# Kernel optimization log

Measured on AMD Instinct MI355X. Metric: run time of the kernel, lower is better.

The kernel has to match this reference:

```python
import jax, jax.numpy as jnp
import numpy as np

H = 128   # hidden_size
C = 80    # number of classes / per-class GRUs


def setup_inputs():
    key = jax.random.key(0)
    ks = jax.random.split(key, 16)
    lengths = np.array([100 + 4 * j for j in range(C)], dtype=np.int64)   # ragged segment sizes
    ucl = np.concatenate([np.zeros(1, np.int64), np.cumsum(lengths)])     # [C+1] boundaries
    N = int(ucl[-1])                                                      # 20640 total boxes
    r = jax.random.normal
    return {
        "boxes_feature": r(ks[0], (N, 1024), jnp.float32),
        "boxes_score": r(ks[1], (N, 32), jnp.float32),
        "boxes_box": r(ks[2], (N, 4), jnp.float32),
        "all_class_boxes_feature": r(ks[3], (N, 1024), jnp.float32),
        "all_class_boxes_score": r(ks[4], (N, 32), jnp.float32),
        "all_class_boxes_box": r(ks[5], (N, 32), jnp.float32),
        "all_class_boxes_origin_score": r(ks[6], (N, 32), jnp.float32),
        "unique_class": np.ones(C, dtype=np.int64),
        "unique_class_len": ucl,
        "appear_W": r(ks[7], (H, 1024), jnp.float32) / np.sqrt(1024.0).astype(np.float32),
        "appear_b": jnp.zeros((H,), jnp.float32),
        "feat_W": r(ks[8], (H, H + 96), jnp.float32) / np.sqrt(float(H + 96)).astype(np.float32),
        "feat_b": jnp.zeros((H,), jnp.float32),
        "gru_Wih": r(ks[9], (C, 2, 3 * H, H), jnp.float32) / np.sqrt(float(H)).astype(np.float32),
        "gru_Whh": r(ks[10], (C, 2, 3 * H, H), jnp.float32) / np.sqrt(float(H)).astype(np.float32),
        "gru_bih": r(ks[11], (C, 2, 3 * H), jnp.float32) * 0.01,
        "gru_bhh": r(ks[12], (C, 2, 3 * H), jnp.float32) * 0.01,
        "out_W": r(ks[13], (1, 2 * H), jnp.float32) / np.sqrt(2.0 * H).astype(np.float32),
        "out_b": jnp.zeros((1,), jnp.float32),
    }


def _forward(all_class_boxes_feature, all_class_boxes_score, all_class_boxes_box,
             all_class_boxes_origin_score, unique_class, unique_class_len,
             appear_W, appear_b, feat_W, feat_b,
             gru_Wih, gru_Whh, gru_bih, gru_bhh, out_W, out_b):
    # --- static ragged bookkeeping (int inputs are concrete numpy) ---
    ucl = np.asarray(unique_class_len)
    lengths = ucl[1:] - ucl[:-1]                                   # [C]
    starts = ucl[:-1]
    L = int(lengths.max())
    t = np.arange(L)
    mask = jnp.asarray(t[None, :] < lengths[:, None])              # [C,L] valid-position mask
    gidx = jnp.asarray(starts[:, None] + np.minimum(t[None, :], lengths[:, None] - 1))  # [C,L]
    ridx = jnp.asarray(np.clip(lengths[:, None] - 1 - t[None, :], 0, None))             # [C,L]

    # --- shared feature pipeline ---
    feat = jax.nn.relu(all_class_boxes_feature @ appear_W.T + appear_b)   # [N,H]
    allf = jnp.concatenate([feat, all_class_boxes_score, all_class_boxes_box,
                            all_class_boxes_origin_score], axis=1)        # [N,H+96]
    dec = jax.nn.relu(allf @ feat_W.T + feat_b)                           # [N,H]

    X = dec[gidx]                                                  # [C,L,H] padded per-class segments
    Xr = jnp.take_along_axis(X, ridx[:, :, None], axis=1)          # time-reversed within each length

    def run_dir(Xd, Wih, Whh, bih, bhh):
        # precompute input projections; scan only carries the hidden recurrence
        Xp = jnp.einsum('clh,cgh->clg', Xd, Wih) + bih[:, None, :]  # [C,L,3H]

        def per_class(xp, m, Whh_c, bhh_c):
            def step(h, inp):
                x_t, m_t = inp
                gh = Whh_c @ h + bhh_c
                r = jax.nn.sigmoid(x_t[:H] + gh[:H])                # PyTorch gate order r,z,n
                z = jax.nn.sigmoid(x_t[H:2 * H] + gh[H:2 * H])
                n = jnp.tanh(x_t[2 * H:] + r * gh[2 * H:])
                h2 = jnp.where(m_t, (1.0 - z) * n + z * h, h)
                return h2, h2
            _, out = jax.lax.scan(step, jnp.zeros((H,), xp.dtype), (xp, m))
            return out                                              # [L,H]
        return jax.vmap(per_class)(Xp, mask, Whh, bhh)              # [C,L,H]

    out_f = run_dir(X, gru_Wih[:, 0], gru_Whh[:, 0], gru_bih[:, 0], gru_bhh[:, 0])
    out_r = run_dir(Xr, gru_Wih[:, 1], gru_Whh[:, 1], gru_bih[:, 1], gru_bhh[:, 1])
    out_bd = jnp.take_along_axis(out_r, ridx[:, :, None], axis=1)   # un-reverse backward outputs
    Y = jnp.concatenate([out_f, out_bd], axis=-1)                   # [C,L,2H]

    # flatten valid positions back to the original box order (segments are contiguous)
    seg = jnp.asarray(np.repeat(np.arange(C), lengths))
    loc = jnp.asarray(np.concatenate([np.arange(int(l)) for l in lengths]))
    flat = Y[seg, loc]                                              # [N,2H]
    return jax.nn.sigmoid(flat @ out_W.T + out_b)[:, None, :]       # [N,1,1] like torch output


def reference(boxes_feature, boxes_score, boxes_box, all_class_boxes_feature,
              all_class_boxes_score, all_class_boxes_box, all_class_boxes_origin_score,
              unique_class, unique_class_len, appear_W, appear_b, feat_W, feat_b,
              gru_Wih, gru_Whh, gru_bih, gru_bhh, out_W, out_b):
    # boxes_feature/boxes_score/boxes_box are accepted but unused, as in the torch forward
    return _forward(all_class_boxes_feature, all_class_boxes_score, all_class_boxes_box,
                    all_class_boxes_origin_score, unique_class, unique_class_len,
                    appear_W, appear_b, feat_W, feat_b,
                    gru_Wih, gru_Whh, gru_bih, gru_bhh, out_W, out_b)
```

## Files before the change

kernel.cpp:

```cpp
#include <hip/hip_runtime.h>
#include <hip/hip_bf16.h>
#include <cstdint>


typedef _Float16 half2_t __attribute__((ext_vector_type(2)));
typedef _Float16 half8_t __attribute__((ext_vector_type(8)));
typedef float f32x4 __attribute__((ext_vector_type(4)));

__device__ __forceinline__ void lds_barrier() {
    asm volatile("s_waitcnt lgkmcnt(0)\n\ts_barrier" ::: "memory");
}

__device__ __forceinline__ half8_t cvt8(float4 f0, float4 f1) {
    return half8_t{(_Float16)f0.x, (_Float16)f0.y, (_Float16)f0.z, (_Float16)f0.w,
                   (_Float16)f1.x, (_Float16)f1.y, (_Float16)f1.z, (_Float16)f1.w};
}

__global__ __launch_bounds__(256) void concat_kernel(
    const float* __restrict__ score, const float* __restrict__ box,
    const float* __restrict__ orig, _Float16* __restrict__ allf, int N)
{
    int idx = blockIdx.x * 256 + threadIdx.x;
    int total = N * 96;
    if (idx >= total) return;
    int n = idx / 96, j = idx - n * 96;
    float v;
    if (j < 32)      v = score[(size_t)n * 32 + j];
    else if (j < 64) v = box  [(size_t)n * 32 + j - 32];
    else             v = orig [(size_t)n * 32 + j - 64];
    allf[(size_t)n * 224 + 128 + j] = (_Float16)v;
}

template<bool A_F16>
__global__ __launch_bounds__(256) void mfma_gemm_kernel(
    const void* __restrict__ Av, int lda,
    const float* __restrict__ B, int ldb,
    const float* __restrict__ bias,
    _Float16* __restrict__ Cc, int ldc,
    int Nrows, int K, int do_relu)
{
    __shared__ __align__(16) _Float16 Asl[256 * 8];
    __shared__ __align__(16) _Float16 Bsl[512 * 8];
    const int tid = threadIdx.x;
    const int wave = tid >> 6, lane = tid & 63;
    const int n0 = blockIdx.x * 64;

    const int a_rt = tid >> 6, a_q = (tid >> 4) & 3, a_m = tid & 15;
    int arow = n0 + a_rt * 16 + a_m; if (arow > Nrows - 1) arow = Nrows - 1;
    const int b_q = (tid >> 4) & 3, b_n = tid & 15;
    const int bcol0 = (tid >> 6) * 16 + b_n;
    const int bcol1 = bcol0 + 64;

    f32x4 acc[8] = {};
    half8_t a_st, b_st0, b_st1;

    auto load_chunk = [&](int kc) {
        int k = kc * 32;
        if constexpr (A_F16) {
            const _Float16* A = (const _Float16*)Av;
            a_st = *(const half8_t*)(A + (size_t)arow * lda + k + a_q * 8);
        } else {
            const float* A = (const float*)Av;
            const float4* p = (const float4*)(A + (size_t)arow * lda + k + a_q * 8);
            a_st = cvt8(p[0], p[1]);
        }
        const float4* p0 = (const float4*)(B + (size_t)bcol0 * ldb + k + b_q * 8);
        const float4* p1 = (const float4*)(B + (size_t)bcol1 * ldb + k + b_q * 8);
        b_st0 = cvt8(p0[0], p0[1]);
        b_st1 = cvt8(p1[0], p1[1]);
    };

    load_chunk(0);
    const int nkc = K >> 5;
    for (int kc = 0; kc < nkc; kc++) {
        lds_barrier();
        *(half8_t*)(Asl + tid * 8) = a_st;
        *(half8_t*)(Bsl + tid * 8) = b_st0;
        *(half8_t*)(Bsl + (tid + 256) * 8) = b_st1;
        lds_barrier();
        if (kc + 1 < nkc) load_chunk(kc + 1);
        half8_t af = *(const half8_t*)(Asl + (wave * 64 + lane) * 8);
        #pragma unroll
        for (int ct = 0; ct < 8; ct++) {
            half8_t bf = *(const half8_t*)(Bsl + (ct * 64 + lane) * 8);
            acc[ct] = __builtin_amdgcn_mfma_f32_16x16x32_f16(af, bf, acc[ct], 0, 0, 0);
        }
    }

    const int crow = n0 + wave * 16 + (lane >> 4) * 4;
    const int ccol = lane & 15;
    #pragma unroll
    for (int ct = 0; ct < 8; ct++) {
        int col = ct * 16 + ccol;
        float bv = bias[col];
        #pragma unroll
        for (int reg = 0; reg < 4; reg++) {
            int row = crow + reg;
            if (row >= Nrows) continue;
            float v = acc[ct][reg] + bv;
            if (do_relu) v = v > 0.f ? v : 0.f;
            Cc[(size_t)row * ldc + col] = (_Float16)v;
        }
    }
}

__global__ __launch_bounds__(256) void mfma_xp_kernel(
    const _Float16* __restrict__ dec,
    const float* __restrict__ Wih,
    const float* __restrict__ bih,
    const int* __restrict__ ucl,
    _Float16* __restrict__ xp,
    int N)
{
    const int c = blockIdx.x;
    const int tile = blockIdx.y;
    const int d = blockIdx.z / 3, mt = blockIdx.z % 3;
    const int start = ucl[c];
    const int len = ucl[c + 1] - start;
    const int t0 = tile * 64;
    if (t0 >= len) return;

    __shared__ __align__(16) _Float16 Asl[256 * 8];
    __shared__ __align__(16) _Float16 Bsl[512 * 8];
    const int tid = threadIdx.x;
    const int wave = tid >> 6, lane = tid & 63;

    const int a_rt = tid >> 6, a_q = (tid >> 4) & 3, a_m = tid & 15;
    int t = t0 + a_rt * 16 + a_m; if (t > len - 1) t = len - 1;
    const int srow = start + (d ? (len - 1 - t) : t);

    const float* Bb = Wih + ((size_t)(c * 2 + d) * 384 + mt * 128) * 128;
    const int b_q = (tid >> 4) & 3, b_n = tid & 15;
    const int bcol0 = (tid >> 6) * 16 + b_n;
    const int bcol1 = bcol0 + 64;

    f32x4 acc[8] = {};
    half8_t a_st, b_st0, b_st1;

    auto load_chunk = [&](int kc) {
        int k = kc * 32;
        a_st = *(const half8_t*)(dec + (size_t)srow * 128 + k + a_q * 8);
        const float4* p0 = (const float4*)(Bb + (size_t)bcol0 * 128 + k + b_q * 8);
        const float4* p1 = (const float4*)(Bb + (size_t)bcol1 * 128 + k + b_q * 8);
        b_st0 = cvt8(p0[0], p0[1]);
        b_st1 = cvt8(p1[0], p1[1]);
    };

    load_chunk(0);
    for (int kc = 0; kc < 4; kc++) {
        lds_barrier();
        *(half8_t*)(Asl + tid * 8) = a_st;
        *(half8_t*)(Bsl + tid * 8) = b_st0;
        *(half8_t*)(Bsl + (tid + 256) * 8) = b_st1;
        lds_barrier();
        if (kc + 1 < 4) load_chunk(kc + 1);
        half8_t af = *(const half8_t*)(Asl + (wave * 64 + lane) * 8);
        #pragma unroll
        for (int ct = 0; ct < 8; ct++) {
            half8_t bf = *(const half8_t*)(Bsl + (ct * 64 + lane) * 8);
            acc[ct] = __builtin_amdgcn_mfma_f32_16x16x32_f16(af, bf, acc[ct], 0, 0, 0);
        }
    }

    const float* bias = bih + (size_t)(c * 2 + d) * 384 + mt * 128;
    const int trow = t0 + wave * 16 + (lane >> 4) * 4;
    const int ccol = lane & 15;
    #pragma unroll
    for (int ct = 0; ct < 8; ct++) {
        int col = ct * 16 + ccol;
        float bv = bias[col];
        #pragma unroll
        for (int reg = 0; reg < 4; reg++) {
            int tt = trow + reg;
            if (tt >= len) continue;
            float v = acc[ct][reg] + bv;
            xp[((size_t)d * N + start + tt) * 384 + mt * 128 + col] = (_Float16)v;
        }
    }
}

__global__ __launch_bounds__(128, 1) void gru_kernel(
    const _Float16* __restrict__ xp,
    const float* __restrict__ Whh,
    const float* __restrict__ bhh,
    const int* __restrict__ ucl,
    float* __restrict__ outY,
    int N)
{
    const int c = blockIdx.x, d = blockIdx.y;
    const int start = ucl[c];
    const int len = ucl[c + 1] - start;
    const int g = threadIdx.x;

    const float* wbase = Whh + (size_t)(c * 2 + d) * 384 * 128;
    half2_t w0[64], w1[64], w2[64];
    {
        const float2* r0 = (const float2*)(wbase + (size_t)g * 128);
        const float2* r1 = (const float2*)(wbase + (size_t)(g + 128) * 128);
        const float2* r2 = (const float2*)(wbase + (size_t)(g + 256) * 128);
        #pragma unroll
        for (int i = 0; i < 64; i++) {
            float2 a = r0[i];
            w0[i] = half2_t{(_Float16)a.x, (_Float16)a.y};
        }
        #pragma unroll
        for (int i = 0; i < 64; i++) {
            float2 a = r1[i];
            w1[i] = half2_t{(_Float16)a.x, (_Float16)a.y};
        }
        #pragma unroll
        for (int i = 0; i < 64; i++) {
            float2 a = r2[i];
            w2[i] = half2_t{(_Float16)a.x, (_Float16)a.y};
        }
    }
    const float* bb = bhh + (size_t)(c * 2 + d) * 384;
    const float bh0 = bb[g], bh1 = bb[g + 128], bh2 = bb[g + 256];

    __shared__ __align__(16) half2_t hbuf[2][64];
    if (g < 64) { hbuf[0][g] = half2_t{(_Float16)0.f, (_Float16)0.f}; }
    const _Float16* xpb = xp + ((size_t)d * N + start) * 384;
    float* outb = outY + (size_t)start * 256 + d * 128;

    float xa0 = (float)xpb[g], xa1 = (float)xpb[g + 128], xa2 = (float)xpb[g + 256];
    const size_t o1 = (size_t)((len > 1) ? 1 : 0) * 384;
    float xb0 = (float)xpb[o1 + g], xb1 = (float)xpb[o1 + g + 128], xb2 = (float)xpb[o1 + g + 256];
    float hcur = 0.f;
    lds_barrier();

#define GRU_SUBSTEP(HP_IDX, HN_IDX, X0, X1, X2, TT)                          \
    {                                                                        \
        const half8_t* __restrict__ hp = (const half8_t*)hbuf[HP_IDX];       \
        _Float16* __restrict__ hn = (_Float16*)hbuf[HN_IDX];                 \
        float a0 = bh0, a1 = bh1, a2 = bh2;                                  \
        half8_t hr[4];                                                       \
        hr[0] = hp[0]; hr[1] = hp[1]; hr[2] = hp[2]; hr[3] = hp[3];          \
        _Pragma("unroll")                                                    \
        for (int i = 0; i < 16; i++) {                                       \
            union { half8_t v; half2_t h2[4]; } u;                           \
            u.v = hr[i & 3];                                                 \
            if (i + 4 < 16) hr[i & 3] = hp[i + 4];                           \
            _Pragma("unroll")                                                \
            for (int j = 0; j < 4; j++) {                                    \
                a0 = __builtin_amdgcn_fdot2(w0[i * 4 + j], u.h2[j], a0, false);\
                a1 = __builtin_amdgcn_fdot2(w1[i * 4 + j], u.h2[j], a1, false);\
                a2 = __builtin_amdgcn_fdot2(w2[i * 4 + j], u.h2[j], a2, false);\
            }                                                                \
        }                                                                    \
        float r = __fdividef(1.f, 1.f + __expf(-((X0) + a0)));               \
        float z = __fdividef(1.f, 1.f + __expf(-((X1) + a1)));               \
        float pre = (X2) + r * a2;                                           \
        float n = 1.f - __fdividef(2.f, __expf(2.f * pre) + 1.f);            \
        float hnew = (1.f - z) * n + z * hcur;                               \
        hn[g] = (_Float16)hnew;                                              \
        hcur = hnew;                                                         \
        outb[(size_t)(TT) * 256 + g] = hnew;                                 \
    }

    for (int t = 0; t < len; t += 2) {
        int tpa = (t + 2 < len) ? (t + 2) : (len - 1);
        const _Float16* xra = xpb + (size_t)tpa * 384;
        float ta0 = (float)xra[g], ta1 = (float)xra[g + 128], ta2 = (float)xra[g + 256];
        int ttA = d ? (len - 1 - t) : t;
        GRU_SUBSTEP(0, 1, xa0, xa1, xa2, ttA)
        xa0 = ta0; xa1 = ta1; xa2 = ta2;
        lds_barrier();
        if (t + 1 >= len) break;
        int tpb = (t + 3 < len) ? (t + 3) : (len - 1);
        const _Float16* xrb = xpb + (size_t)tpb * 384;
        float tb0 = (float)xrb[g], tb1 = (float)xrb[g + 128], tb2 = (float)xrb[g + 256];
        int ttB = d ? (len - 2 - t) : (t + 1);
        GRU_SUBSTEP(1, 0, xb0, xb1, xb2, ttB)
        xb0 = tb0; xb1 = tb1; xb2 = tb2;
        lds_barrier();
    }
#undef GRU_SUBSTEP
}

__global__ __launch_bounds__(256) void final_kernel(
    const float* __restrict__ outY,
    const float* __restrict__ outW,
    const float* __restrict__ outb,
    float* __restrict__ out, int N)
{
    __shared__ __align__(16) float wsh[256];
    wsh[threadIdx.x] = outW[threadIdx.x];
    __syncthreads();
    const int lane = threadIdx.x & 63;
    const int wave = (blockIdx.x * 256 + threadIdx.x) >> 6;
    const int nw = gridDim.x * 4;
    float4 w4 = *(const float4*)&wsh[lane * 4];
    float b = outb[0];
    for (int n = wave; n < N; n += nw) {
        float4 y = *(const float4*)(outY + (size_t)n * 256 + lane * 4);
        float p = y.x * w4.x + y.y * w4.y + y.z * w4.z + y.w * w4.w;
        #pragma unroll
        for (int off = 32; off > 0; off >>= 1) p += __shfl_down(p, off);
        if (lane == 0) out[n] = 1.f / (1.f + __expf(-(p + b)));
    }
}

extern "C" void kernel_launch(void* const* d_in, const int* in_sizes, int n_in,
                              void* d_out, int out_size, void* d_ws, size_t ws_size,
                              hipStream_t stream)
{
    const float* acbf  = (const float*)d_in[3];
    const float* score = (const float*)d_in[4];
    const float* box   = (const float*)d_in[5];
    const float* orig  = (const float*)d_in[6];
    const int*   ucl   = (const int*)d_in[8];
    const float* aW  = (const float*)d_in[9];
    const float* ab  = (const float*)d_in[10];
    const float* fW  = (const float*)d_in[11];
    const float* fb  = (const float*)d_in[12];
    const float* Wih = (const float*)d_in[13];
    const float* Whh = (const float*)d_in[14];
    const float* bih = (const float*)d_in[15];
    const float* bhh = (const float*)d_in[16];
    const float* oW  = (const float*)d_in[17];
    const float* ob  = (const float*)d_in[18];
    float* out = (float*)d_out;

    const int N = in_sizes[3] / 1024;
    const int C = in_sizes[7];

    _Float16* allf16 = (_Float16*)d_ws;
    _Float16* dec16  = allf16 + (size_t)N * 224;
    _Float16* xp16   = dec16 + (size_t)N * 128;
    float*    outY   = (float*)(xp16 + (size_t)2 * N * 384);

    dim3 blk(256);
    const int rowblocks = (N + 63) / 64;
    concat_kernel<<<dim3((N * 96 + 255) / 256), blk, 0, stream>>>(score, box, orig, allf16, N);
    mfma_gemm_kernel<false><<<dim3(rowblocks), blk, 0, stream>>>(
        (const void*)acbf, 1024, aW, 1024, ab, allf16, 224, N, 1024, 1);
    mfma_gemm_kernel<true><<<dim3(rowblocks), blk, 0, stream>>>(
        (const void*)allf16, 224, fW, 224, fb, dec16, 128, N, 224, 1);
    mfma_xp_kernel<<<dim3(C, 7, 6), blk, 0, stream>>>(dec16, Wih, bih, ucl, xp16, N);
    gru_kernel<<<dim3(C, 2), dim3(128), 0, stream>>>(xp16, Whh, bhh, ucl, outY, N);
    final_kernel<<<dim3(160), blk, 0, stream>>>(outY, oW, ob, out, N);
}
```

Baseline: 610.3 us.

## Stage GRU input projections into LDS in double-buffered chunks via async loads

The recurrent GRU kernel now prefetches 32-timestep chunks of the precomputed input projections into a double-buffered LDS area using global_load_lds, instead of issuing per-step global loads into registers. The hidden-state dot products are split into two independent accumulator chains, and all 16 h vectors are loaded up front, to shorten the dependency chain on each serial step. The aim is to take global memory latency off the latency-bound recurrence. The cost is extra LDS use, a vmcnt wait plus barrier at each chunk boundary, and possibly more register pressure.

```diff
diff --git a/kernel.cpp b/kernel.cpp
--- a/kernel.cpp
+++ b/kernel.cpp
@@ -9,6 +9,12 @@
 
 __device__ __forceinline__ void lds_barrier() {
     asm volatile("s_waitcnt lgkmcnt(0)\n\ts_barrier" ::: "memory");
+}
+
+__device__ __forceinline__ void gload_lds16(const _Float16* g, _Float16* l) {
+    __builtin_amdgcn_global_load_lds(
+        (const __attribute__((address_space(1))) void*)g,
+        (__attribute__((address_space(3))) void*)l, 16, 0, 0);
 }
 
 __device__ __forceinline__ half8_t cvt8(float4 f0, float4 f1) {
@@ -179,6 +185,7 @@
     }
 }
 
+#define XCH 32
 __global__ __launch_bounds__(128, 1) void gru_kernel(
     const _Float16* __restrict__ xp,
     const float* __restrict__ Whh,
@@ -191,6 +198,28 @@
     const int start = ucl[c];
     const int len = ucl[c + 1] - start;
     const int g = threadIdx.x;
+    const int wave = g >> 6, lane = g & 63;
+
+    __shared__ __align__(16) _Float16 xs[2][XCH * 384];
+    __shared__ __align__(16) half2_t hbuf[2][64];
+
+    const _Float16* xpb = xp + ((size_t)d * N + start) * 384;
+    const int slice = len * 384;
+
+    auto stage_chunk = [&](int ch) {
+        const int base = ch * (XCH * 384);
+        _Float16* lb = (_Float16*)xs[ch & 1];
+        #pragma unroll
+        for (int i = 0; i < 12; i++) {
+            const int slot = wave * 12 + i;
+            int off = base + slot * 512 + lane * 8;
+            const int mx = slice - 8;
+            if (off > mx) off = mx;
+            gload_lds16(xpb + off, lb + slot * 512);
+        }
+    };
+
+    stage_chunk(0);
 
     const float* wbase = Whh + (size_t)(c * 2 + d) * 384 * 128;
     half2_t w0[64], w1[64], w2[64];
@@ -217,65 +246,64 @@
     const float* bb = bhh + (size_t)(c * 2 + d) * 384;
     const float bh0 = bb[g], bh1 = bb[g + 128], bh2 = bb[g + 256];
 
-    __shared__ __align__(16) half2_t hbuf[2][64];
     if (g < 64) { hbuf[0][g] = half2_t{(_Float16)0.f, (_Float16)0.f}; }
-    const _Float16* xpb = xp + ((size_t)d * N + start) * 384;
+    float hcur = 0.f;
     float* outb = outY + (size_t)start * 256 + d * 128;
 
-    float xa0 = (float)xpb[g], xa1 = (float)xpb[g + 128], xa2 = (float)xpb[g + 256];
-    const size_t o1 = (size_t)((len > 1) ? 1 : 0) * 384;
-    float xb0 = (float)xpb[o1 + g], xb1 = (float)xpb[o1 + g + 128], xb2 = (float)xpb[o1 + g + 256];
-    float hcur = 0.f;
-    lds_barrier();
-
-#define GRU_SUBSTEP(HP_IDX, HN_IDX, X0, X1, X2, TT)                          \
-    {                                                                        \
-        const half8_t* __restrict__ hp = (const half8_t*)hbuf[HP_IDX];       \
-        _Float16* __restrict__ hn = (_Float16*)hbuf[HN_IDX];                 \
-        float a0 = bh0, a1 = bh1, a2 = bh2;                                  \
-        half8_t hr[4];                                                       \
-        hr[0] = hp[0]; hr[1] = hp[1]; hr[2] = hp[2]; hr[3] = hp[3];          \
-        _Pragma("unroll")                                                    \
-        for (int i = 0; i < 16; i++) {                                       \
-            union { half8_t v; half2_t h2[4]; } u;                           \
-            u.v = hr[i & 3];                                                 \
-            if (i + 4 < 16) hr[i & 3] = hp[i + 4];                           \
-            _Pragma("unroll")                                                \
-            for (int j = 0; j < 4; j++) {                                    \
-                a0 = __builtin_amdgcn_fdot2(w0[i * 4 + j], u.h2[j], a0, false);\
-                a1 = __builtin_amdgcn_fdot2(w1[i * 4 + j], u.h2[j], a1, false);\
-                a2 = __builtin_amdgcn_fdot2(w2[i * 4 + j], u.h2[j], a2, false);\
-            }                                                                \
-        }                                                                    \
-        float r = __fdividef(1.f, 1.f + __expf(-((X0) + a0)));               \
-        float z = __fdividef(1.f, 1.f + __expf(-((X1) + a1)));               \
-        float pre = (X2) + r * a2;                                           \
-        float n = 1.f - __fdividef(2.f, __expf(2.f * pre) + 1.f);            \
-        float hnew = (1.f - z) * n + z * hcur;                               \
-        hn[g] = (_Float16)hnew;                                              \
-        hcur = hnew;                                                         \
-        outb[(size_t)(TT) * 256 + g] = hnew;                                 \
-    }
-
-    for (int t = 0; t < len; t += 2) {
-        int tpa = (t + 2 < len) ? (t + 2) : (len - 1);
-        const _Float16* xra = xpb + (size_t)tpa * 384;
-        float ta0 = (float)xra[g], ta1 = (float)xra[g + 128], ta2 = (float)xra[g + 256];
-        int ttA = d ? (len - 1 - t) : t;
-        GRU_SUBSTEP(0, 1, xa0, xa1, xa2, ttA)
-        xa0 = ta0; xa1 = ta1; xa2 = ta2;
-        lds_barrier();
-        if (t + 1 >= len) break;
-        int tpb = (t + 3 < len) ? (t + 3) : (len - 1);
-        const _Float16* xrb = xpb + (size_t)tpb * 384;
-        float tb0 = (float)xrb[g], tb1 = (float)xrb[g + 128], tb2 = (float)xrb[g + 256];
-        int ttB = d ? (len - 2 - t) : (t + 1);
-        GRU_SUBSTEP(1, 0, xb0, xb1, xb2, ttB)
-        xb0 = tb0; xb1 = tb1; xb2 = tb2;
-        lds_barrier();
-    }
-#undef GRU_SUBSTEP
-}
+    asm volatile("s_waitcnt vmcnt(0) lgkmcnt(0)\n\ts_barrier" ::: "memory");
+
+    const int nch = (len + XCH - 1) / XCH;
+    if (nch > 1) stage_chunk(1);
+
+    int t = 0;
+    for (int ch = 0; ch < nch; ch++) {
+        const _Float16* xc = (const _Float16*)xs[ch & 1];
+        const int rem = len - ch * XCH;
+        const int tend = rem < XCH ? rem : XCH;
+        for (int tm = 0; tm < tend; tm++, t++) {
+            float x0 = (float)xc[tm * 384 + g];
+            float x1 = (float)xc[tm * 384 + 128 + g];
+            float x2 = (float)xc[tm * 384 + 256 + g];
+            const half8_t* __restrict__ hp = (const half8_t*)hbuf[t & 1];
+            half8_t h8[16];
+            #pragma unroll
+            for (int i = 0; i < 16; i++) h8[i] = hp[i];
+            float a0 = bh0, a1 = bh1, a2 = bh2;
+            float b0 = 0.f, b1 = 0.f, b2 = 0.f;
+            #pragma unroll
+            for (int i = 0; i < 8; i++) {
+                union { half8_t v; half2_t h2[4]; } u, v2;
+                u.v = h8[i]; v2.v = h8[i + 8];
+                #pragma unroll
+                for (int j = 0; j < 4; j++) {
+                    a0 = __builtin_amdgcn_fdot2(w0[i * 4 + j],      u.h2[j],  a0, false);
+                    b0 = __builtin_amdgcn_fdot2(w0[32 + i * 4 + j], v2.h2[j], b0, false);
+                    a1 = __builtin_amdgcn_fdot2(w1[i * 4 + j],      u.h2[j],  a1, false);
+                    b1 = __builtin_amdgcn_fdot2(w1[32 + i * 4 + j], v2.h2[j], b1, false);
+                    a2 = __builtin_amdgcn_fdot2(w2[i * 4 + j],      u.h2[j],  a2, false);
+                    b2 = __builtin_amdgcn_fdot2(w2[32 + i * 4 + j], v2.h2[j], b2, false);
+                }
+            }
+            a0 += b0; a1 += b1; a2 += b2;
+            float r = __fdividef(1.f, 1.f + __expf(-(x0 + a0)));
+            float z = __fdividef(1.f, 1.f + __expf(-(x1 + a1)));
+            float pre = x2 + r * a2;
+            float n = 1.f - __fdividef(2.f, __expf(2.f * pre) + 1.f);
+            float hnew = (1.f - z) * n + z * hcur;
+            ((_Float16*)hbuf[(t + 1) & 1])[g] = (_Float16)hnew;
+            hcur = hnew;
+            int tt = d ? (len - 1 - t) : t;
+            outb[(size_t)tt * 256 + g] = hnew;
+            lds_barrier();
+        }
+        if (ch + 1 < nch) {
+            asm volatile("s_waitcnt vmcnt(0)" ::: "memory");
+            __builtin_amdgcn_s_barrier();
+            if (ch + 2 < nch) stage_chunk(ch + 2);
+        }
+    }
+}
+#undef XCH
 
 __global__ __launch_bounds__(256) void final_kernel(
     const float* __restrict__ outY,
```

After: 631.1 us. +3.4%, slower.

## Run GRU recurrence in a single wave using readlane broadcast instead of LDS

Applied to the files above, without the earlier changes.

The GRU kernel now uses one 64-lane wave per (class, direction), each lane owning two hidden units and holding six weight rows (384 half2 registers). The hidden state is exchanged through v_readlane broadcasts instead of an LDS buffer with barriers. Weight pairs are repacked as (k, k+64) so lane i's packed hidden value pairs with column i and i+64. This removes the per-step LDS round trip and s_barrier but doubles per-thread FMA work and register pressure, which may cause spills.

```diff
diff --git a/kernel.cpp b/kernel.cpp
--- a/kernel.cpp
+++ b/kernel.cpp
@@ -179,7 +179,7 @@
     }
 }
 
-__global__ __launch_bounds__(128, 1) void gru_kernel(
+__global__ __launch_bounds__(64, 1) void gru_kernel(
     const _Float16* __restrict__ xp,
     const float* __restrict__ Whh,
     const float* __restrict__ bhh,
@@ -190,91 +190,86 @@
     const int c = blockIdx.x, d = blockIdx.y;
     const int start = ucl[c];
     const int len = ucl[c + 1] - start;
-    const int g = threadIdx.x;
+    const int l = threadIdx.x;
 
     const float* wbase = Whh + (size_t)(c * 2 + d) * 384 * 128;
-    half2_t w0[64], w1[64], w2[64];
-    {
-        const float2* r0 = (const float2*)(wbase + (size_t)g * 128);
-        const float2* r1 = (const float2*)(wbase + (size_t)(g + 128) * 128);
-        const float2* r2 = (const float2*)(wbase + (size_t)(g + 256) * 128);
-        #pragma unroll
-        for (int i = 0; i < 64; i++) {
-            float2 a = r0[i];
-            w0[i] = half2_t{(_Float16)a.x, (_Float16)a.y};
-        }
-        #pragma unroll
-        for (int i = 0; i < 64; i++) {
-            float2 a = r1[i];
-            w1[i] = half2_t{(_Float16)a.x, (_Float16)a.y};
-        }
-        #pragma unroll
-        for (int i = 0; i < 64; i++) {
-            float2 a = r2[i];
-            w2[i] = half2_t{(_Float16)a.x, (_Float16)a.y};
-        }
-    }
+
+    half2_t wR0[64], wZ0[64], wN0[64], wR1[64], wZ1[64], wN1[64];
+#define LOADROW(arr, row)                                                     \
+    {                                                                         \
+        const float2* ra = (const float2*)(wbase + (size_t)(row) * 128);      \
+        const float2* rb = ra + 32;                                           \
+        _Pragma("unroll")                                                     \
+        for (int i2 = 0; i2 < 32; i2++) {                                     \
+            float2 fa = ra[i2], fb = rb[i2];                                  \
+            arr[i2 * 2 + 0] = half2_t{(_Float16)fa.x, (_Float16)fb.x};        \
+            arr[i2 * 2 + 1] = half2_t{(_Float16)fa.y, (_Float16)fb.y};        \
+        }                                                                     \
+    }
+    LOADROW(wR0, l)
+    LOADROW(wZ0, l + 128)
+    LOADROW(wN0, l + 256)
+    LOADROW(wR1, l + 64)
+    LOADROW(wZ1, l + 192)
+    LOADROW(wN1, l + 320)
+#undef LOADROW
+
     const float* bb = bhh + (size_t)(c * 2 + d) * 384;
-    const float bh0 = bb[g], bh1 = bb[g + 128], bh2 = bb[g + 256];
-
-    __shared__ __align__(16) half2_t hbuf[2][64];
-    if (g < 64) { hbuf[0][g] = half2_t{(_Float16)0.f, (_Float16)0.f}; }
+    const float bR0 = bb[l],      bZ0 = bb[l + 128], bN0 = bb[l + 256];
+    const float bR1 = bb[l + 64], bZ1 = bb[l + 192], bN1 = bb[l + 320];
+
     const _Float16* xpb = xp + ((size_t)d * N + start) * 384;
     float* outb = outY + (size_t)start * 256 + d * 128;
 
-    float xa0 = (float)xpb[g], xa1 = (float)xpb[g + 128], xa2 = (float)xpb[g + 256];
-    const size_t o1 = (size_t)((len > 1) ? 1 : 0) * 384;
-    float xb0 = (float)xpb[o1 + g], xb1 = (float)xpb[o1 + g + 128], xb2 = (float)xpb[o1 + g + 256];
-    float hcur = 0.f;
-    lds_barrier();
-
-#define GRU_SUBSTEP(HP_IDX, HN_IDX, X0, X1, X2, TT)                          \
-    {                                                                        \
-        const half8_t* __restrict__ hp = (const half8_t*)hbuf[HP_IDX];       \
-        _Float16* __restrict__ hn = (_Float16*)hbuf[HN_IDX];                 \
-        float a0 = bh0, a1 = bh1, a2 = bh2;                                  \
-        half8_t hr[4];                                                       \
-        hr[0] = hp[0]; hr[1] = hp[1]; hr[2] = hp[2]; hr[3] = hp[3];          \
-        _Pragma("unroll")                                                    \
-        for (int i = 0; i < 16; i++) {                                       \
-            union { half8_t v; half2_t h2[4]; } u;                           \
-            u.v = hr[i & 3];                                                 \
-            if (i + 4 < 16) hr[i & 3] = hp[i + 4];                           \
-            _Pragma("unroll")                                                \
-            for (int j = 0; j < 4; j++) {                                    \
-                a0 = __builtin_amdgcn_fdot2(w0[i * 4 + j], u.h2[j], a0, false);\
-                a1 = __builtin_amdgcn_fdot2(w1[i * 4 + j], u.h2[j], a1, false);\
-                a2 = __builtin_amdgcn_fdot2(w2[i * 4 + j], u.h2[j], a2, false);\
-            }                                                                \
-        }                                                                    \
-        float r = __fdividef(1.f, 1.f + __expf(-((X0) + a0)));               \
-        float z = __fdividef(1.f, 1.f + __expf(-((X1) + a1)));               \
-        float pre = (X2) + r * a2;                                           \
-        float n = 1.f - __fdividef(2.f, __expf(2.f * pre) + 1.f);            \
-        float hnew = (1.f - z) * n + z * hcur;                               \
-        hn[g] = (_Float16)hnew;                                              \
-        hcur = hnew;                                                         \
-        outb[(size_t)(TT) * 256 + g] = hnew;                                 \
-    }
-
-    for (int t = 0; t < len; t += 2) {
-        int tpa = (t + 2 < len) ? (t + 2) : (len - 1);
-        const _Float16* xra = xpb + (size_t)tpa * 384;
-        float ta0 = (float)xra[g], ta1 = (float)xra[g + 128], ta2 = (float)xra[g + 256];
-        int ttA = d ? (len - 1 - t) : t;
-        GRU_SUBSTEP(0, 1, xa0, xa1, xa2, ttA)
-        xa0 = ta0; xa1 = ta1; xa2 = ta2;
-        lds_barrier();
-        if (t + 1 >= len) break;
-        int tpb = (t + 3 < len) ? (t + 3) : (len - 1);
-        const _Float16* xrb = xpb + (size_t)tpb * 384;
-        float tb0 = (float)xrb[g], tb1 = (float)xrb[g + 128], tb2 = (float)xrb[g + 256];
-        int ttB = d ? (len - 2 - t) : (t + 1);
-        GRU_SUBSTEP(1, 0, xb0, xb1, xb2, ttB)
-        xb0 = tb0; xb1 = tb1; xb2 = tb2;
-        lds_barrier();
-    }
-#undef GRU_SUBSTEP
+    float xr0 = (float)xpb[l],      xz0 = (float)xpb[128 + l], xn0 = (float)xpb[256 + l];
+    float xr1 = (float)xpb[64 + l], xz1 = (float)xpb[192 + l], xn1 = (float)xpb[320 + l];
+
+    float hA = 0.f, hB = 0.f;
+    int hvi = 0;
+
+    for (int t = 0; t < len; t++) {
+        int tn = (t + 1 < len) ? (t + 1) : t;
+        const _Float16* xt = xpb + (size_t)tn * 384;
+        float pr0 = (float)xt[l],      pz0 = (float)xt[128 + l], pn0 = (float)xt[256 + l];
+        float pr1 = (float)xt[64 + l], pz1 = (float)xt[192 + l], pn1 = (float)xt[320 + l];
+
+        float aR0 = bR0, aZ0 = bZ0, aN0 = bN0;
+        float aR1 = bR1, aZ1 = bZ1, aN1 = bN1;
+        #pragma unroll
+        for (int i = 0; i < 64; i++) {
+            int hb = __builtin_amdgcn_readlane(hvi, i);
+            half2_t h2 = __builtin_bit_cast(half2_t, hb);
+            aR0 = __builtin_amdgcn_fdot2(wR0[i], h2, aR0, false);
+            aZ0 = __builtin_amdgcn_fdot2(wZ0[i], h2, aZ0, false);
+            aN0 = __builtin_amdgcn_fdot2(wN0[i], h2, aN0, false);
+            aR1 = __builtin_amdgcn_fdot2(wR1[i], h2, aR1, false);
+            aZ1 = __builtin_amdgcn_fdot2(wZ1[i], h2, aZ1, false);
+            aN1 = __builtin_amdgcn_fdot2(wN1[i], h2, aN1, false);
+        }
+
+        float rA = __fdividef(1.f, 1.f + __expf(-(xr0 + aR0)));
+        float zA = __fdividef(1.f, 1.f + __expf(-(xz0 + aZ0)));
+        float preA = xn0 + rA * aN0;
+        float nA = 1.f - __fdividef(2.f, __expf(2.f * preA) + 1.f);
+        float hnA = (1.f - zA) * nA + zA * hA;
+
+        float rB = __fdividef(1.f, 1.f + __expf(-(xr1 + aR1)));
+        float zB = __fdividef(1.f, 1.f + __expf(-(xz1 + aZ1)));
+        float preB = xn1 + rB * aN1;
+        float nB = 1.f - __fdividef(2.f, __expf(2.f * preB) + 1.f);
+        float hnB = (1.f - zB) * nB + zB * hB;
+
+        hA = hnA; hB = hnB;
+        half2_t hh{(_Float16)hA, (_Float16)hB};
+        hvi = __builtin_bit_cast(int, hh);
+
+        int tt = d ? (len - 1 - t) : t;
+        outb[(size_t)tt * 256 + l] = hA;
+        outb[(size_t)tt * 256 + 64 + l] = hB;
+
+        xr0 = pr0; xz0 = pz0; xn0 = pn0;
+        xr1 = pr1; xz1 = pz1; xn1 = pn1;
+    }
 }
 
 __global__ __launch_bounds__(256) void final_kernel(
@@ -337,6 +332,6 @@
     mfma_gemm_kernel<true><<<dim3(rowblocks), blk, 0, stream>>>(
         (const void*)allf16, 224, fW, 224, fb, dec16, 128, N, 224, 1);
     mfma_xp_kernel<<<dim3(C, 7, 6), blk, 0, stream>>>(dec16, Wih, bih, ucl, xp16, N);
-    gru_kernel<<<dim3(C, 2), dim3(128), 0, stream>>>(xp16, Whh, bhh, ucl, outY, N);
+    gru_kernel<<<dim3(C, 2), dim3(64), 0, stream>>>(xp16, Whh, bhh, ucl, outY, N);
     final_kernel<<<dim3(160), blk, 0, stream>>>(outY, oW, ob, out, N);
 }
```

Measured after the change: 920.5 us. 1.51x slower.
